# Optimization experiments

Hardware: AMD Instinct MI355X
Metric: run time of the kernel (lower is better)

The kernel has to match this reference:

```python
import jax, jax.numpy as jnp
import numpy as np

BATCH, NUM_MASKS, IN_DIM, OUT_DIM = 512, 16, 1024, 1024


def setup_inputs() -> dict:
    key = jax.random.key(0)
    k1, k2, k3 = jax.random.split(key, 3)
    x = jax.random.normal(k1, (BATCH, NUM_MASKS, IN_DIM), dtype=jnp.float32)
    kernel = jax.random.normal(k2, (IN_DIM, OUT_DIM), dtype=jnp.float32) * (1.0 / np.sqrt(IN_DIM))
    masks = jax.random.uniform(k3, (NUM_MASKS, IN_DIM, OUT_DIM), dtype=jnp.float32)
    return {"x": x, "kernel": kernel, "masks": masks}


def reference(x, kernel, masks):
    # masked_kernel[m, i, o] = kernel[i, o] * masks[m, i, o]
    masked_kernel = kernel[None, :, :] * masks  # (M, I, O)
    # Original tf.scan serializes batch; equivalent math is one batched einsum:
    # out[b, m, o] = sum_i x[b, m, i] * masked_kernel[m, i, o]
    # NOTE: the executed tf.scan path applies NO activation, so neither do we.
    out = jnp.einsum('bmi,mio->bmo', x, masked_kernel)  # (B, M, O)
    return out
```

## Files before the change

### kernel.cpp

```cpp
#include <hip/hip_runtime.h>
#include <hip/hip_bf16.h>


#define BATCH 512
#define NMASK 16
#define IN_D  1024
#define OUT_D 1024

#define BM 128
#define BN 128
#define BK 32
#define NT (IN_D / BK)
#define AKP 40
#define BKP 34
#define THREADS 512

using bf16x8  = __attribute__((ext_vector_type(8))) __bf16;
using bf16x4t = __attribute__((ext_vector_type(4))) __bf16;
using f32x4   = __attribute__((ext_vector_type(4))) float;
using f32x2   = __attribute__((ext_vector_type(2))) float;
using u16x8   = __attribute__((ext_vector_type(8))) unsigned short;
using u16x4   = __attribute__((ext_vector_type(4))) unsigned short;

__device__ __forceinline__ unsigned short f2bf(float f) {
    unsigned u = __float_as_uint(f);
    u += 0x7fffu + ((u >> 16) & 1u);
    return (unsigned short)(u >> 16);
}

struct BRegs { f32x2 kv[4]; f32x2 mv[4]; };

__global__ void __launch_bounds__(THREADS, 4)
mdl_mfma_kernel(const float* __restrict__ X,
                const float* __restrict__ Kn,
                const float* __restrict__ Mk,
                float* __restrict__ Out)
{
    __shared__ __align__(16) unsigned short As[2][BM * AKP];
    __shared__ __align__(16) unsigned short Bs[2][BN * BKP];

    const int t = threadIdx.x;
    const int l = t & 63;
    const int w = t >> 6;

    const int raw = blockIdx.x;
    const int wg  = (raw & 7) * 64 + (raw >> 3);
    const int m   = wg >> 5;
    const int ob  = (wg >> 2) & 7;
    const int bb  = wg & 3;

    const int wr = w >> 2;
    const int wc = w & 3;

    f32x4 acc[4][2];
#pragma unroll
    for (int mi = 0; mi < 4; ++mi)
#pragma unroll
        for (int ni = 0; ni < 2; ++ni)
            acc[mi][ni] = (f32x4){0.f, 0.f, 0.f, 0.f};

    const int a_row = t >> 2;
    const int a_k   = (t & 3) * 8;
    const int o_l = (t & 63) * 2;
    const int ig  = t >> 6;
    const int i_l = ig * 4;

    const float* Xa  = X + ((size_t)(bb * BM + a_row) * NMASK + m) * IN_D + a_k;
    const float* Knb = Kn + (size_t)i_l * OUT_D + ob * BN + o_l;
    const float* Mkb = Mk + ((size_t)m * IN_D + i_l) * OUT_D + ob * BN + o_l;

    f32x4 av0, av1;
    BRegs b0, b1;

    auto LOADA = [&](int kt) {
        av0 = *(const f32x4*)(Xa + kt);
        av1 = *(const f32x4*)(Xa + kt + 4);
    };
    auto LOADB = [&](BRegs& bg, int kt) {
#pragma unroll
        for (int r = 0; r < 4; ++r) {
            bg.kv[r] = *(const f32x2*)(Knb + (size_t)(kt + r) * OUT_D);
            bg.mv[r] = *(const f32x2*)(Mkb + (size_t)(kt + r) * OUT_D);
        }
    };
    auto STORE = [&](int buf, BRegs& bg) {
#pragma unroll
        for (int c = 0; c < 2; ++c) {
            u16x4 v;
#pragma unroll
            for (int r = 0; r < 4; ++r) v[r] = f2bf(bg.kv[r][c] * bg.mv[r][c]);
            *(u16x4*)(&Bs[buf][(o_l + c) * BKP + ig * 4]) = v;
        }
        u16x8 va;
#pragma unroll
        for (int j = 0; j < 4; ++j) { va[j] = f2bf(av0[j]); va[4 + j] = f2bf(av1[j]); }
        *(u16x8*)(&As[buf][a_row * AKP + a_k]) = va;
    };
    auto MFMA_PHASE = [&](int buf) {
        const int kg = (l >> 4) * 8;
        bf16x8 bfv[2];
#pragma unroll
        for (int ni = 0; ni < 2; ++ni) {
            const int n = wc * 32 + ni * 16 + (l & 15);
            bf16x4t lo = *(const bf16x4t*)(&Bs[buf][n * BKP + kg]);
            bf16x4t hi = *(const bf16x4t*)(&Bs[buf][n * BKP + kg + 4]);
            bf16x8 f;
            f[0] = lo[0]; f[1] = lo[1]; f[2] = lo[2]; f[3] = lo[3];
            f[4] = hi[0]; f[5] = hi[1]; f[6] = hi[2]; f[7] = hi[3];
            bfv[ni] = f;
        }
#pragma unroll
        for (int mi = 0; mi < 4; ++mi) {
            const int r = wr * 64 + mi * 16 + (l & 15);
            bf16x8 af = *(const bf16x8*)(&As[buf][r * AKP + kg]);
#pragma unroll
            for (int ni = 0; ni < 2; ++ni)
                acc[mi][ni] = __builtin_amdgcn_mfma_f32_16x16x32_bf16(
                    af, bfv[ni], acc[mi][ni], 0, 0, 0);
        }
    };
    auto BARRIER = [&]() {
        asm volatile("s_waitcnt lgkmcnt(0)" ::: "memory");
        __builtin_amdgcn_sched_barrier(0);
        __builtin_amdgcn_s_barrier();
        __builtin_amdgcn_sched_barrier(0);
    };

    LOADA(0);
    LOADB(b0, 0);
    STORE(0, b0);
    LOADB(b1, BK);
    BARRIER();

    for (int tt = 0; tt < NT; tt += 2) {
        if (tt + 1 < NT) LOADA((tt + 1) * BK);
        if (tt + 2 < NT) LOADB(b0, (tt + 2) * BK);
        __builtin_amdgcn_sched_barrier(0);
        MFMA_PHASE(0);
        if (tt + 1 < NT) STORE(1, b1);
        BARRIER();
        if (tt + 2 < NT) LOADA((tt + 2) * BK);
        if (tt + 3 < NT) LOADB(b1, (tt + 3) * BK);
        __builtin_amdgcn_sched_barrier(0);
        MFMA_PHASE(1);
        if (tt + 2 < NT) STORE(0, b0);
        BARRIER();
    }

    const int r0 = bb * BM + wr * 64 + (l >> 4) * 4;
    const int c0 = ob * BN + wc * 32 + (l & 15);
#pragma unroll
    for (int mi = 0; mi < 4; ++mi) {
#pragma unroll
        for (int j = 0; j < 4; ++j) {
            const size_t row = (size_t)(r0 + mi * 16 + j);
            float* op = Out + (row * NMASK + m) * OUT_D + c0;
#pragma unroll
            for (int ni = 0; ni < 2; ++ni)
                op[ni * 16] = acc[mi][ni][j];
        }
    }
}

extern "C" void kernel_launch(void* const* d_in, const int* in_sizes, int n_in,
                              void* d_out, int out_size, void* d_ws, size_t ws_size,
                              hipStream_t stream) {
    (void)in_sizes; (void)n_in; (void)d_ws; (void)ws_size; (void)out_size;
    const float* X  = (const float*)d_in[0];
    const float* Kn = (const float*)d_in[1];
    const float* Mk = (const float*)d_in[2];
    float* Out = (float*)d_out;

    const int nblocks = (BATCH / BM) * (OUT_D / BN) * NMASK;
    mdl_mfma_kernel<<<nblocks, THREADS, 0, stream>>>(X, Kn, Mk, Out);
}
```

Baseline: 56.90 us.

## Halve N tile to 64 with 256 threads, swizzle B LDS, native bf16 cast

Shrinks the output tile from 128x128 to 128x64 and the block to 256 threads (4 waves), which doubles the grid and remaps the block-to-(mask, out-block, batch-block) swizzle. Each thread now loads 16 contiguous X floats per k-step. The B tile in LDS uses an XOR swizzle of 4-element groups keyed on the output column to reduce bank conflicts on the transposed stores and fragment reads. The hand-written round-to-nearest bf16 conversion is replaced by the native __bf16 cast, so the compiler can use hardware convert instructions. The smaller N tile means X is re-read twice as often, in exchange for more blocks and more parallelism.

Result: slower. 72.43 us (+27.3%).

```diff
diff --git a/kernel.cpp b/kernel.cpp
--- a/kernel.cpp
+++ b/kernel.cpp
@@ -8,27 +8,21 @@
 #define OUT_D 1024
 
 #define BM 128
-#define BN 128
+#define BN 64
 #define BK 32
 #define NT (IN_D / BK)
 #define AKP 40
 #define BKP 34
-#define THREADS 512
+#define THREADS 256
 
-using bf16x8  = __attribute__((ext_vector_type(8))) __bf16;
-using bf16x4t = __attribute__((ext_vector_type(4))) __bf16;
-using f32x4   = __attribute__((ext_vector_type(4))) float;
-using f32x2   = __attribute__((ext_vector_type(2))) float;
-using u16x8   = __attribute__((ext_vector_type(8))) unsigned short;
-using u16x4   = __attribute__((ext_vector_type(4))) unsigned short;
-
-__device__ __forceinline__ unsigned short f2bf(float f) {
-    unsigned u = __float_as_uint(f);
-    u += 0x7fffu + ((u >> 16) & 1u);
-    return (unsigned short)(u >> 16);
-}
+using bf16x8 = __attribute__((ext_vector_type(8))) __bf16;
+using bf16x4 = __attribute__((ext_vector_type(4))) __bf16;
+using f32x4  = __attribute__((ext_vector_type(4))) float;
+using f32x2  = __attribute__((ext_vector_type(2))) float;
 
 struct BRegs { f32x2 kv[4]; f32x2 mv[4]; };
+
+__device__ __forceinline__ int physg(int g, int o) { return g ^ (o & 7); }
 
 __global__ void __launch_bounds__(THREADS, 4)
 mdl_mfma_kernel(const float* __restrict__ X,
@@ -44,13 +38,13 @@
     const int w = t >> 6;
 
     const int raw = blockIdx.x;
-    const int wg  = (raw & 7) * 64 + (raw >> 3);
-    const int m   = wg >> 5;
-    const int ob  = (wg >> 2) & 7;
+    const int wg  = (raw & 7) * 128 + (raw >> 3);
+    const int m   = wg >> 6;
+    const int ob  = (wg >> 2) & 15;
     const int bb  = wg & 3;
 
-    const int wr = w >> 2;
-    const int wc = w & 3;
+    const int wr = w >> 1;
+    const int wc = w & 1;
 
     f32x4 acc[4][2];
 #pragma unroll
@@ -59,22 +53,23 @@
         for (int ni = 0; ni < 2; ++ni)
             acc[mi][ni] = (f32x4){0.f, 0.f, 0.f, 0.f};
 
-    const int a_row = t >> 2;
-    const int a_k   = (t & 3) * 8;
-    const int o_l = (t & 63) * 2;
-    const int ig  = t >> 6;
+    const int a_row = t >> 1;
+    const int a_kh  = (t & 1) * 16;
+    const int o_l = (t & 31) * 2;
+    const int ig  = t >> 5;
     const int i_l = ig * 4;
 
-    const float* Xa  = X + ((size_t)(bb * BM + a_row) * NMASK + m) * IN_D + a_k;
+    const float* Xa  = X + ((size_t)(bb * BM + a_row) * NMASK + m) * IN_D + a_kh;
     const float* Knb = Kn + (size_t)i_l * OUT_D + ob * BN + o_l;
     const float* Mkb = Mk + ((size_t)m * IN_D + i_l) * OUT_D + ob * BN + o_l;
 
-    f32x4 av0, av1;
+    f32x4 av[4];
     BRegs b0, b1;
 
     auto LOADA = [&](int kt) {
-        av0 = *(const f32x4*)(Xa + kt);
-        av1 = *(const f32x4*)(Xa + kt + 4);
+#pragma unroll
+        for (int j = 0; j < 4; ++j)
+            av[j] = *(const f32x4*)(Xa + kt + j * 4);
     };
     auto LOADB = [&](BRegs& bg, int kt) {
 #pragma unroll
@@ -86,24 +81,31 @@
     auto STORE = [&](int buf, BRegs& bg) {
 #pragma unroll
         for (int c = 0; c < 2; ++c) {
-            u16x4 v;
+            const int o = o_l + c;
+            bf16x4 v;
 #pragma unroll
-            for (int r = 0; r < 4; ++r) v[r] = f2bf(bg.kv[r][c] * bg.mv[r][c]);
-            *(u16x4*)(&Bs[buf][(o_l + c) * BKP + ig * 4]) = v;
+            for (int r = 0; r < 4; ++r)
+                v[r] = (__bf16)(bg.kv[r][c] * bg.mv[r][c]);
+            *(bf16x4*)(&Bs[buf][o * BKP + physg(ig, o) * 4]) = v;
         }
-        u16x8 va;
+        bf16x8 va0, va1;
 #pragma unroll
-        for (int j = 0; j < 4; ++j) { va[j] = f2bf(av0[j]); va[4 + j] = f2bf(av1[j]); }
-        *(u16x8*)(&As[buf][a_row * AKP + a_k]) = va;
+        for (int j = 0; j < 4; ++j) {
+            va0[j]     = (__bf16)av[0][j];  va0[4 + j] = (__bf16)av[1][j];
+            va1[j]     = (__bf16)av[2][j];  va1[4 + j] = (__bf16)av[3][j];
+        }
+        *(bf16x8*)(&As[buf][a_row * AKP + a_kh])     = va0;
+        *(bf16x8*)(&As[buf][a_row * AKP + a_kh + 8]) = va1;
     };
     auto MFMA_PHASE = [&](int buf) {
         const int kg = (l >> 4) * 8;
+        const int Gb = (l >> 4) * 2;
         bf16x8 bfv[2];
 #pragma unroll
         for (int ni = 0; ni < 2; ++ni) {
             const int n = wc * 32 + ni * 16 + (l & 15);
-            bf16x4t lo = *(const bf16x4t*)(&Bs[buf][n * BKP + kg]);
-            bf16x4t hi = *(const bf16x4t*)(&Bs[buf][n * BKP + kg + 4]);
+            bf16x4 lo = *(const bf16x4*)(&Bs[buf][n * BKP + physg(Gb, n) * 4]);
+            bf16x4 hi = *(const bf16x4*)(&Bs[buf][n * BKP + physg(Gb + 1, n) * 4]);
             bf16x8 f;
             f[0] = lo[0]; f[1] = lo[1]; f[2] = lo[2]; f[3] = lo[3];
             f[4] = hi[0]; f[5] = hi[1]; f[6] = hi[2]; f[7] = hi[3];
```
